# Optimization experiments

Hardware: AMD Instinct MI355X
Metric: run time of the kernel (lower is better)

## Reference

```python
import jax, jax.numpy as jnp
import numpy as np

N = 65536       # active voxels
C = 128         # embed_channels
DEPTH = 4
NSEG = 1024     # number of clusters per level
K = 27          # 3x3x3 kernel taps
LRELU = 0.01
EPS_BN = 1e-5


def _bn(x, g, b):
    # training-mode batchnorm over the voxel axis (biased variance, as torch)
    m = jnp.mean(x, axis=0)
    v = jnp.var(x, axis=0)
    return (x - m) * jax.lax.rsqrt(v + EPS_BN) * g + b


def _lrelu(x):
    return jnp.where(x >= 0, x, LRELU * x)


def _proj(x, w, g, b):
    # Linear(bias=False) -> BatchNorm1d -> LeakyReLU
    return _lrelu(_bn(x @ w, g, b))


def setup_inputs() -> dict:
    key = jax.random.key(0)
    ks = jax.random.split(key, 24)
    s = 1.0 / np.sqrt(C)
    sc = 1.0 / np.sqrt(K * C)
    u = lambda k, shp, sk: jax.random.uniform(k, shp, jnp.float32, -sk, sk)
    g = lambda k, shp: 1.0 + 0.1 * jax.random.normal(k, shp, jnp.float32)
    inp = {}
    inp['feat'] = jax.random.normal(ks[0], (N, C), jnp.float32)
    inp['clusters'] = jax.random.randint(ks[1], (DEPTH - 1, N), 0, NSEG)
    # neighbor table for 3x3x3 sparse conv; value == N means neighbor absent
    inp['neighbor_idx'] = jax.random.randint(ks[2], (N, K), 0, N + 1)
    inp['lw_w'] = u(ks[3], (DEPTH - 1, C, C), s)
    inp['lw_gamma'] = g(ks[4], (DEPTH - 1, C))
    inp['lw_beta'] = 0.1 * jax.random.normal(ks[5], (DEPTH - 1, C), jnp.float32)
    inp['w_w'] = u(ks[6], (DEPTH - 1, C, C), s)
    inp['proj_w'] = u(ks[7], (DEPTH, C, C), s)
    inp['proj_gamma'] = g(ks[8], (DEPTH, C))
    inp['proj_beta'] = 0.1 * jax.random.normal(ks[9], (DEPTH, C), jnp.float32)
    inp['adaptive_w'] = u(ks[10], (C, DEPTH - 1), s)
    inp['fuse_w'] = u(ks[11], (2 * C, C), 1.0 / np.sqrt(2 * C))
    inp['fuse_gamma'] = g(ks[12], (C,))
    inp['fuse_beta'] = 0.1 * jax.random.normal(ks[13], (C,), jnp.float32)
    inp['conv1_w'] = u(ks[14], (K, C, C), sc)
    inp['conv2_w'] = u(ks[15], (K, C, C), sc)
    inp['bn1_gamma'] = g(ks[16], (C,))
    inp['bn1_beta'] = 0.1 * jax.random.normal(ks[17], (C,), jnp.float32)
    inp['bn2_gamma'] = g(ks[18], (C,))
    inp['bn2_beta'] = 0.1 * jax.random.normal(ks[19], (C,), jnp.float32)
    return inp


def _forward(feat, clusters, neighbor_idx, lw_w, lw_gamma, lw_beta, w_w,
             proj_w, proj_gamma, proj_beta, adaptive_w, fuse_w, fuse_gamma,
             fuse_beta, conv1_w, conv2_w, bn1_gamma, bn1_beta, bn2_gamma,
             bn2_beta):
    x_in = feat
    feats = []
    for i in range(DEPTH - 1):
        c = clusters[i]
        pw = _proj(feat, lw_w[i], lw_gamma[i], lw_beta[i])          # [N,C]
        cnt = jnp.maximum(
            jax.ops.segment_sum(jnp.ones((N,), feat.dtype), c, num_segments=NSEG), 1.0)
        seg_mean = jax.ops.segment_sum(pw, c, num_segments=NSEG) / cnt[:, None]
        pw = pw - seg_mean[c]                                        # center per cluster
        pw = pw @ w_w[i]
        pw = jnp.exp(pw - jnp.max(pw))                               # global max, as in source
        pw = pw / (jax.ops.segment_sum(pw, c, num_segments=NSEG)[c] + 1e-6)
        pf = _proj(feat, proj_w[i], proj_gamma[i], proj_beta[i]) * pw
        feats.append(jax.ops.segment_sum(pf, c, num_segments=NSEG)[c])
    adp = jax.nn.softmax(feat @ adaptive_w, axis=1)                  # [N,3]
    feats = jnp.stack(feats, axis=1)                                 # [N,3,C]
    agg = jnp.einsum('ld,ldc->lc', adp, feats)                       # [N,C]
    f_last = _proj(feat, proj_w[DEPTH - 1], proj_gamma[DEPTH - 1], proj_beta[DEPTH - 1])
    fused = _proj(jnp.concatenate([f_last, agg], axis=1), fuse_w, fuse_gamma, fuse_beta) + x_in
    residual = fused
    # 3x3x3 sparse conv on fixed topology: 27 masked gathers + per-tap GEMM
    mask = (neighbor_idx < N).astype(fused.dtype)                    # [N,K]
    idx = jnp.minimum(neighbor_idx, N - 1)

    def sconv(x, w):
        out = jnp.zeros((N, C), x.dtype)
        for k in range(K):
            out = out + (jnp.take(x, idx[:, k], axis=0) * mask[:, k:k + 1]) @ w[k]
        return out

    d = _lrelu(_bn(sconv(fused, conv1_w), bn1_gamma, bn1_beta))
    d = _lrelu(_bn(sconv(d, conv2_w), bn2_gamma, bn2_beta) + residual)
    return d


def reference(feat, clusters, neighbor_idx, lw_w, lw_gamma, lw_beta, w_w,
              proj_w, proj_gamma, proj_beta, adaptive_w, fuse_w, fuse_gamma,
              fuse_beta, conv1_w, conv2_w, bn1_gamma, bn1_beta, bn2_gamma,
              bn2_beta):
    return _forward(feat, clusters, neighbor_idx, lw_w, lw_gamma, lw_beta,
                    w_w, proj_w, proj_gamma, proj_beta, adaptive_w, fuse_w,
                    fuse_gamma, fuse_beta, conv1_w, conv2_w, bn1_gamma,
                    bn1_beta, bn2_gamma, bn2_beta)
```

## Files before the change

### kernel.cpp

```cpp
#include <hip/hip_runtime.h>

typedef unsigned short u16;
typedef unsigned int u32;
typedef __attribute__((ext_vector_type(8))) short bf16x8;
typedef __attribute__((ext_vector_type(4))) float f32x4;
typedef __attribute__((ext_vector_type(4))) u32 u32x4;

#define NROWS 65536
#define CCH 128
#define PE ((size_t)65537*128)

__device__ __forceinline__ float bf2f(u16 x){ u32 u=((u32)x)<<16; return __builtin_bit_cast(float,u); }
__device__ __forceinline__ u16 f2bf(float f){ u32 u=__builtin_bit_cast(u32,f); u += 0x7fffu + ((u>>16)&1u); return (u16)(u>>16); }
__device__ __forceinline__ float lrelu(float v){ return v>=0.f? v : 0.01f*v; }
__device__ __forceinline__ u32 fenc(float f){ u32 u=__builtin_bit_cast(u32,f); return (u & 0x80000000u) ? ~u : (u | 0x80000000u); }
__device__ __forceinline__ float fdec(u32 u){ u32 b = (u & 0x80000000u) ? (u ^ 0x80000000u) : ~u; return __builtin_bit_cast(float,b); }

__global__ __launch_bounds__(256) void prep_transpose(
    const float* __restrict__ lw, const float* __restrict__ ww, const float* __restrict__ pj,
    const float* __restrict__ fw, const float* __restrict__ c1, const float* __restrict__ c2,
    u16* __restrict__ WT)
{
  int i = blockIdx.x*256 + threadIdx.x;
  float v;
  if (i < 49152)      { int j=i;        int m=j>>14,e=j&16383,n=e>>7,k=e&127; v=lw[(m<<14)+(k<<7)+n]; }
  else if (i < 98304) { int j=i-49152;  int m=j>>14,e=j&16383,n=e>>7,k=e&127; v=ww[(m<<14)+(k<<7)+n]; }
  else if (i < 163840){ int j=i-98304;  int m=j>>14,e=j&16383,n=e>>7,k=e&127; v=pj[(m<<14)+(k<<7)+n]; }
  else if (i < 196608){ int j=i-163840; int n=j>>8, k=j&255;                  v=fw[(k<<7)+n]; }
  else if (i < 638976){ int j=i-196608; int m=j>>14,e=j&16383,n=e>>7,k=e&127; v=c1[(m<<14)+(k<<7)+n]; }
  else                { int j=i-638976; int m=j>>14,e=j&16383,n=e>>7,k=e&127; v=c2[(m<<14)+(k<<7)+n]; }
  WT[i]=f2bf(v);
}

__global__ __launch_bounds__(256) void nbrT_k(const int* __restrict__ nbr, int* __restrict__ nbrT){
  __shared__ int s[64*27];
  int b = blockIdx.x;
  for (int i=threadIdx.x; i<64*27; i+=256) s[i] = nbr[b*64*27 + i];
  __syncthreads();
  for (int i=threadIdx.x; i<64*27; i+=256){
    int tap=i>>6, row=i&63;
    nbrT[(size_t)tap*NROWS + b*64 + row] = s[row*27 + tap];
  }
}

__global__ __launch_bounds__(256) void hist_k(const int* __restrict__ cl, int* __restrict__ cnt){
  int i = blockIdx.x*256 + threadIdx.x;
  int l = i>>16;
  atomicAdd(&cnt[l*1024 + cl[i]], 1);
}
__global__ __launch_bounds__(1024) void scan_k(const int* __restrict__ cnt, int* __restrict__ starts, int* __restrict__ cur){
  int l = blockIdx.x, t = threadIdx.x;
  __shared__ int s[1024];
  int v = cnt[l*1024+t];
  s[t]=v; __syncthreads();
  for (int off=1; off<1024; off<<=1){
    int u_ = (t>=off) ? s[t-off] : 0;
    __syncthreads();
    s[t] += u_;
    __syncthreads();
  }
  int incl=s[t], excl=incl-v;
  starts[l*1025+t]=excl;
  if (t==1023) starts[l*1025+1024]=incl;
  cur[l*1024+t]=excl;
}
__global__ __launch_bounds__(256) void scatter_k(const int* __restrict__ cl, int* __restrict__ cur, int* __restrict__ order){
  int i = blockIdx.x*256 + threadIdx.x;
  int l = i>>16;
  int c = cl[i];
  int p = atomicAdd(&cur[l*1024+c], 1);
  order[l*65536 + p] = i & 65535;
}

struct BS7 { const u16* BT[7]; u16* out[7]; float* stats[7]; };

__global__ __launch_bounds__(256,2) void gemm_feat7(const float* __restrict__ feat, BS7 p)
{
  const int tid=threadIdx.x, lane=tid&63, quad=lane>>4, l15=lane&15;
  const int w=tid>>6, rh=w>>1, chq=w&1;
  const int row0=blockIdx.x*128;

  __shared__ __align__(16) u16 ldsA[128*136];
  __shared__ float cs[256];

  #pragma unroll
  for (int it=0; it<8; ++it){
    int row = it*16 + (tid>>4), chn = tid&15;
    const float* Af = feat + (size_t)(row0+row)*CCH + chn*8;
    float4 lo = *(const float4*)(Af);
    float4 hi = *(const float4*)(Af+4);
    u32x4 d;
    d[0]=(u32)f2bf(lo.x)|((u32)f2bf(lo.y)<<16);
    d[1]=(u32)f2bf(lo.z)|((u32)f2bf(lo.w)<<16);
    d[2]=(u32)f2bf(hi.x)|((u32)f2bf(hi.y)<<16);
    d[3]=(u32)f2bf(hi.z)|((u32)f2bf(hi.w)<<16);
    *(u32x4*)(&ldsA[row*136 + chn*8]) = d;
  }
  __syncthreads();

  #pragma unroll 1
  for (int y=0; y<7; ++y){
    const u16* Bb = p.BT[y];
    f32x4 acc[4][4];
    #pragma unroll
    for (int a_=0;a_<4;++a_)
      #pragma unroll
      for (int b_=0;b_<4;++b_) acc[a_][b_]=(f32x4){0.f,0.f,0.f,0.f};
    #pragma unroll
    for (int ks=0; ks<4; ++ks){
      bf16x8 af[4], bfv[4];
      #pragma unroll
      for (int mb=0;mb<4;++mb)
        af[mb]=*(const bf16x8*)(&ldsA[(rh*64+mb*16+l15)*136 + ks*32 + quad*8]);
      #pragma unroll
      for (int nb=0;nb<4;++nb)
        bfv[nb]=*(const bf16x8*)(Bb + (size_t)(chq*64+nb*16+l15)*CCH + ks*32 + quad*8);
      #pragma unroll
      for (int mb=0;mb<4;++mb)
        #pragma unroll
        for (int nb=0;nb<4;++nb)
          acc[mb][nb]=__builtin_amdgcn_mfma_f32_16x16x32_bf16(af[mb],bfv[nb],acc[mb][nb],0,0,0);
    }
    u16* O = p.out[y];
    #pragma unroll
    for (int mb=0;mb<4;++mb){
      int rbase=row0+rh*64+mb*16+quad*4;
      #pragma unroll
      for (int e=0;e<4;++e)
        #pragma unroll
        for (int nb=0;nb<4;++nb)
          O[(size_t)(rbase+e)*CCH + chq*64+nb*16+l15]=f2bf(acc[mb][nb][e]);
    }
    __syncthreads();
    cs[tid]=0.f;
    __syncthreads();
    #pragma unroll
    for (int nb=0;nb<4;++nb){
      float s=0.f,s2=0.f;
      #pragma unroll
      for (int mb=0;mb<4;++mb)
        #pragma unroll
        for (int e=0;e<4;++e){ float v=acc[mb][nb][e]; s+=v; s2+=v*v; }
      s += __shfl_xor(s,16);  s += __shfl_xor(s,32);
      s2+= __shfl_xor(s2,16); s2+= __shfl_xor(s2,32);
      if (lane<16){
        int col=chq*64+nb*16+l15;
        atomicAdd(&cs[col],s); atomicAdd(&cs[128+col],s2);
      }
    }
    __syncthreads();
    atomicAdd(&p.stats[y][tid], cs[tid]);
  }
}

__global__ __launch_bounds__(256) void seg_sum_all(
    const u16* __restrict__ pbase, const float* __restrict__ stats,
    const float* __restrict__ gamma, const float* __restrict__ beta,
    const int* __restrict__ starts, const int* __restrict__ order,
    u16* __restrict__ segmean)
{
  __shared__ float sc[128], sh[128], ssum[128];
  const int tid=threadIdx.x, b=blockIdx.x;
  const int level=b>>10, seg=b&1023;
  const u16* praw = pbase + (size_t)level*PE;
  const float* st = stats + level*256;
  if (tid<128){
    float s=st[tid], s2=st[128+tid];
    float mean=s*(1.0f/65536.0f);
    float var =s2*(1.0f/65536.0f)-mean*mean;
    float rstd=rsqrtf(var+1e-5f);
    float scv =gamma[level*128+tid]*rstd;
    sc[tid]=scv; sh[tid]=beta[level*128+tid]-mean*scv;
    ssum[tid]=0.f;
  }
  __syncthreads();
  const int s0=starts[level*1025+seg], en=starts[level*1025+seg+1];
  const int c2=tid&63, half=tid>>6;
  const int* ord = order + level*65536;
  const float sc0=sc[2*c2], sc1=sc[2*c2+1], sh0=sh[2*c2], sh1=sh[2*c2+1];
  float a0=0.f, a1=0.f;
  for (int m=s0+half; m<en; m+=4){
    int r=ord[m];
    u32 x=*(const u32*)(praw + (size_t)r*CCH + 2*c2);
    a0 += lrelu(sc0*bf2f((u16)(x&0xffffu))+sh0);
    a1 += lrelu(sc1*bf2f((u16)(x>>16))    +sh1);
  }
  atomicAdd(&ssum[2*c2],a0); atomicAdd(&ssum[2*c2+1],a1);
  __syncthreads();
  if (tid<128){
    float inv = 1.0f/fmaxf((float)(en-s0),1.0f);
    segmean[(size_t)b*128+tid]=f2bf(ssum[tid]*inv);
  }
}

__global__ __launch_bounds__(256,2) void gemm_mean(
    const u16* __restrict__ segmean, const u16* __restrict__ wwT, u16* __restrict__ segW)
{
  const int tid=threadIdx.x, lane=tid&63, quad=lane>>4, l15=lane&15;
  const int w=tid>>6, rh=w>>1, chq=w&1;
  const int row0=blockIdx.x*128;
  const int level=row0>>10;
  __shared__ __align__(16) u16 ldsA[128*136];
  #pragma unroll
  for (int it=0; it<8; ++it){
    int row = it*16 + (tid>>4), chn = tid&15;
    *(u32x4*)(&ldsA[row*136 + chn*8]) = *(const u32x4*)(segmean + (size_t)(row0+row)*CCH + chn*8);
  }
  __syncthreads();
  const u16* Bb = wwT + level*16384;
  f32x4 acc[4][4];
  #pragma unroll
  for (int a_=0;a_<4;++a_)
    #pragma unroll
    for (int b_=0;b_<4;++b_) acc[a_][b_]=(f32x4){0.f,0.f,0.f,0.f};
  #pragma unroll
  for (int ks=0; ks<4; ++ks){
    bf16x8 af[4], bfv[4];
    #pragma unroll
    for (int mb=0;mb<4;++mb)
      af[mb]=*(const bf16x8*)(&ldsA[(rh*64+mb*16+l15)*136 + ks*32 + quad*8]);
    #pragma unroll
    for (int nb=0;nb<4;++nb)
      bfv[nb]=*(const bf16x8*)(Bb + (size_t)(chq*64+nb*16+l15)*CCH + ks*32 + quad*8);
    #pragma unroll
    for (int mb=0;mb<4;++mb)
      #pragma unroll
      for (int nb=0;nb<4;++nb)
        acc[mb][nb]=__builtin_amdgcn_mfma_f32_16x16x32_bf16(af[mb],bfv[nb],acc[mb][nb],0,0,0);
  }
  #pragma unroll
  for (int mb=0;mb<4;++mb){
    int rbase=row0+rh*64+mb*16+quad*4;
    #pragma unroll
    for (int e=0;e<4;++e)
      #pragma unroll
      for (int nb=0;nb<4;++nb)
        segW[(size_t)(rbase+e)*CCH + chq*64+nb*16+l15]=f2bf(acc[mb][nb][e]);
  }
}

struct LG { const u16* A[3]; float* out[3]; };
__global__ __launch_bounds__(256,2) void gemm_logits(
    LG p, const u16* __restrict__ wwT,
    const float* __restrict__ stats, const float* __restrict__ lwg, const float* __restrict__ lwb,
    const int* __restrict__ clusters, const u16* __restrict__ segW,
    u32* __restrict__ gmax)
{
  const int tid=threadIdx.x, lane=tid&63, quad=lane>>4, l15=lane&15;
  const int w=tid>>6, rh=w>>1, chq=w&1;
  const int row0=blockIdx.x*128;
  const int y=blockIdx.y;

  __shared__ __align__(16) u16 ldsA[128*136];
  __shared__ float tsc[128], tsh[128];
  __shared__ float wred[4];

  if (tid<128){
    const float* st = stats + y*256;
    float s=st[tid], s2=st[128+tid];
    float mean=s*(1.0f/65536.0f);
    float var =s2*(1.0f/65536.0f)-mean*mean;
    float rstd=rsqrtf(var+1e-5f);
    float scv =lwg[y*128+tid]*rstd;
    tsc[tid]=scv; tsh[tid]=lwb[y*128+tid]-mean*scv;
  }
  __syncthreads();

  const u16* Ab = p.A[y];
  #pragma unroll
  for (int it=0; it<8; ++it){
    int row = it*16 + (tid>>4), chn = tid&15;
    u32x4 d = *(const u32x4*)(Ab + (size_t)(row0+row)*CCH + chn*8);
    #pragma unroll
    for (int pq=0;pq<4;++pq){
      u32 xv=d[pq]; int k=chn*8+2*pq;
      float f0=lrelu(tsc[k  ]*bf2f((u16)(xv&0xffffu))+tsh[k  ]);
      float f1=lrelu(tsc[k+1]*bf2f((u16)(xv>>16))    +tsh[k+1]);
      d[pq]=(u32)f2bf(f0)|((u32)f2bf(f1)<<16);
    }
    *(u32x4*)(&ldsA[row*136 + chn*8]) = d;
  }
  __syncthreads();

  const u16* Bb = wwT + y*16384;
  f32x4 acc[4][4];
  #pragma unroll
  for (int a_=0;a_<4;++a_)
    #pragma unroll
    for (int b_=0;b_<4;++b_) acc[a_][b_]=(f32x4){0.f,0.f,0.f,0.f};
  #pragma unroll
  for (int ks=0; ks<4; ++ks){
    bf16x8 af[4], bfv[4];
    #pragma unroll
    for (int mb=0;mb<4;++mb)
      af[mb]=*(const bf16x8*)(&ldsA[(rh*64+mb*16+l15)*136 + ks*32 + quad*8]);
    #pragma unroll
    for (int nb=0;nb<4;++nb)
      bfv[nb]=*(const bf16x8*)(Bb + (size_t)(chq*64+nb*16+l15)*CCH + ks*32 + quad*8);
    #pragma unroll
    for (int mb=0;mb<4;++mb)
      #pragma unroll
      for (int nb=0;nb<4;++nb)
        acc[mb][nb]=__builtin_amdgcn_mfma_f32_16x16x32_bf16(af[mb],bfv[nb],acc[mb][nb],0,0,0);
  }
  float* O = p.out[y];
  float m=-3.0e38f;
  #pragma unroll
  for (int mb=0;mb<4;++mb){
    int rbase=row0+rh*64+mb*16+quad*4;
    #pragma unroll
    for (int e=0;e<4;++e){
      int row=rbase+e;
      int cl=clusters[(size_t)y*NROWS + row];
      const u16* sw = segW + ((size_t)(y*1024+cl))*CCH;
      #pragma unroll
      for (int nb=0;nb<4;++nb){
        int col=chq*64+nb*16+l15;
        float v=acc[mb][nb][e]-bf2f(sw[col]);
        O[(size_t)row*CCH + col]=v;
        m=fmaxf(m,v);
      }
    }
  }
  #pragma unroll
  for (int o=1;o<64;o<<=1) m=fmaxf(m,__shfl_xor(m,o));
  if (lane==0) wred[w]=m;
  __syncthreads();
  if (tid==0){
    float mm=fmaxf(fmaxf(wred[0],wred[1]),fmaxf(wred[2],wred[3]));
    atomicMax(&gmax[y], fenc(mm));
  }
}

__global__ __launch_bounds__(256,2) void gemm_fuse(
    const u16* __restrict__ A0, const u16* __restrict__ A1,
    const float* __restrict__ tstat, const float* __restrict__ tg, const float* __restrict__ tb,
    const u16* __restrict__ BT, u16* __restrict__ out, float* __restrict__ stats)
{
  const int tid=threadIdx.x, lane=tid&63, quad=lane>>4, l15=lane&15;
  const int w=tid>>6, rh=w>>1, chq=w&1;
  const int row0=blockIdx.x*128;

  __shared__ __align__(16) u16 ldsA[128*136];
  __shared__ float tsc[128], tsh[128];
  __shared__ float cs[256];

  if (tid<128){
    float s=tstat[tid], s2=tstat[128+tid];
    float mean=s*(1.0f/65536.0f);
    float var =s2*(1.0f/65536.0f)-mean*mean;
    float rstd=rsqrtf(var+1e-5f);
    float scv =tg[tid]*rstd;
    tsc[tid]=scv; tsh[tid]=tb[tid]-mean*scv;
  }

  f32x4 acc[4][4];
  #pragma unroll
  for (int a_=0;a_<4;++a_)
    #pragma unroll
    for (int b_=0;b_<4;++b_) acc[a_][b_]=(f32x4){0.f,0.f,0.f,0.f};

  #pragma unroll 1
  for (int tap=0; tap<2; ++tap){
    __syncthreads();
    const u16* Ab = tap ? A1 : A0;
    #pragma unroll
    for (int it=0; it<8; ++it){
      int row = it*16 + (tid>>4), chn = tid&15;
      u32x4 d = *(const u32x4*)(Ab + (size_t)(row0+row)*CCH + chn*8);
      if (tap==0){
        #pragma unroll
        for (int pq=0;pq<4;++pq){
          u32 xv=d[pq]; int k=chn*8+2*pq;
          float f0=lrelu(tsc[k  ]*bf2f((u16)(xv&0xffffu))+tsh[k  ]);
          float f1=lrelu(tsc[k+1]*bf2f((u16)(xv>>16))    +tsh[k+1]);
          d[pq]=(u32)f2bf(f0)|((u32)f2bf(f1)<<16);
        }
      }
      *(u32x4*)(&ldsA[row*136 + chn*8]) = d;
    }
    __syncthreads();
    const u16* Bb = BT + tap*128;
    #pragma unroll
    for (int ks=0; ks<4; ++ks){
      bf16x8 af[4], bfv[4];
      #pragma unroll
      for (int mb=0;mb<4;++mb)
        af[mb]=*(const bf16x8*)(&ldsA[(rh*64+mb*16+l15)*136 + ks*32 + quad*8]);
      #pragma unroll
      for (int nb=0;nb<4;++nb)
        bfv[nb]=*(const bf16x8*)(Bb + (size_t)(chq*64+nb*16+l15)*256 + ks*32 + quad*8);
      #pragma unroll
      for (int mb=0;mb<4;++mb)
        #pragma unroll
        for (int nb=0;nb<4;++nb)
          acc[mb][nb]=__builtin_amdgcn_mfma_f32_16x16x32_bf16(af[mb],bfv[nb],acc[mb][nb],0,0,0);
    }
  }
  #pragma unroll
  for (int mb=0;mb<4;++mb){
    int rbase=row0+rh*64+mb*16+quad*4;
    #pragma unroll
    for (int e=0;e<4;++e)
      #pragma unroll
      for (int nb=0;nb<4;++nb)
        out[(size_t)(rbase+e)*CCH + chq*64+nb*16+l15]=f2bf(acc[mb][nb][e]);
  }
  __syncthreads();
  cs[tid]=0.f;
  __syncthreads();
  #pragma unroll
  for (int nb=0;nb<4;++nb){
    float s=0.f,s2=0.f;
    #pragma unroll
    for (int mb=0;mb<4;++mb)
      #pragma unroll
      for (int e=0;e<4;++e){ float v=acc[mb][nb][e]; s+=v; s2+=v*v; }
    s += __shfl_xor(s,16);  s += __shfl_xor(s,32);
    s2+= __shfl_xor(s2,16); s2+= __shfl_xor(s2,32);
    if (lane<16){
      int col=chq*64+nb*16+l15;
      atomicAdd(&cs[col],s); atomicAdd(&cs[128+col],s2);
    }
  }
  __syncthreads();
  atomicAdd(&stats[tid], cs[tid]);
}

template<bool TRANSA>
__device__ __forceinline__ u32x4 conv_xf(u32x4 d, int ar, int schn,
                                         const float* tsc, const float* tsh)
{
  if (TRANSA){
    if (ar >= NROWS) return (u32x4){0u,0u,0u,0u};
    #pragma unroll
    for (int p=0;p<4;++p){
      u32 xv=d[p]; int k=schn*8+2*p;
      float f0=lrelu(tsc[k  ]*bf2f((u16)(xv&0xffffu))+tsh[k  ]);
      float f1=lrelu(tsc[k+1]*bf2f((u16)(xv>>16))    +tsh[k+1]);
      d[p]=(u32)f2bf(f0)|((u32)f2bf(f1)<<16);
    }
  }
  return d;
}

template<bool TRANSA>
__device__ __forceinline__ void conv_tap(
    int tap, int cur,
    const u16* __restrict__ A, const u16* __restrict__ BT, const int* __restrict__ nbrT,
    int row0, int srow, int schn, int rh, int chq, int quad, int l15,
    u16 (&bufA)[2][128*136],
    u32x4 (&preC)[8], int (&ixC)[8], u32x4 (&preN)[8], int (&ixN)[8],
    f32x4 (&acc)[4][4], const float* tsc, const float* tsh)
{
  if (tap < 25){
    #pragma unroll
    for (int it=0; it<8; ++it){
      int ar = nbrT[(size_t)(tap+2)*NROWS + row0 + it*16 + srow];
      ixN[it]=ar;
      preN[it] = *(const u32x4*)(A + (size_t)ar*CCH + schn*8);
    }
  }
  const u16* Bb = BT + tap*16384;
  #pragma unroll
  for (int ks=0; ks<4; ++ks){
    bf16x8 af[4], bfv[4];
    #pragma unroll
    for (int mb=0;mb<4;++mb)
      af[mb]=*(const bf16x8*)(&bufA[cur][(rh*64+mb*16+l15)*136 + ks*32 + quad*8]);
    #pragma unroll
    for (int nb=0;nb<4;++nb)
      bfv[nb]=*(const bf16x8*)(Bb + (size_t)(chq*64+nb*16+l15)*CCH + ks*32 + quad*8);
    #pragma unroll
    for (int mb=0;mb<4;++mb)
      #pragma unroll
      for (int nb=0;nb<4;++nb)
        acc[mb][nb]=__builtin_amdgcn_mfma_f32_16x16x32_bf16(af[mb],bfv[nb],acc[mb][nb],0,0,0);
  }
  if (tap < 26){
    const int nxt = cur^1;
    #pragma unroll
    for (int it=0; it<8; ++it)
      *(u32x4*)(&bufA[nxt][(it*16+srow)*136 + schn*8]) = conv_xf<TRANSA>(preC[it], ixC[it], schn, tsc, tsh);
  }
  __syncthreads();
}

template<bool TRANSA>
__global__ __launch_bounds__(256,2) void conv_k(
    const u16* __restrict__ A, const u16* __restrict__ BT,
    const int* __restrict__ nbrT, u16* __restrict__ out, float* __restrict__ stats,
    const float* __restrict__ tstat, const float* __restrict__ tg, const float* __restrict__ tb)
{
  const int tid=threadIdx.x, lane=tid&63, quad=lane>>4, l15=lane&15;
  const int w=tid>>6, rh=w>>1, chq=w&1;
  const int row0=blockIdx.x*128;
  const int srow=tid>>4, schn=tid&15;

  __shared__ __align__(16) u16 bufA[2][128*136];
  __shared__ float cs[256];
  __shared__ float tsc[128], tsh[128];

  if (TRANSA){
    if (tid<128){
      float s=tstat[tid], s2=tstat[128+tid];
      float mean=s*(1.0f/65536.0f);
      float var =s2*(1.0f/65536.0f)-mean*mean;
      float rstd=rsqrtf(var+1e-5f);
      float scv =tg[tid]*rstd;
      tsc[tid]=scv; tsh[tid]=tb[tid]-mean*scv;
    }
    __syncthreads();
  }

  u32x4 pre0[8], pre1[8];
  int   ix0[8],  ix1[8];

  {
    u32x4 t0[8]; int i0[8];
    #pragma unroll
    for (int it=0; it<8; ++it){
      i0[it] = nbrT[row0 + it*16 + srow];
      t0[it] = *(const u32x4*)(A + (size_t)i0[it]*CCH + schn*8);
    }
    #pragma unroll
    for (int it=0; it<8; ++it){
      ix0[it] = nbrT[(size_t)NROWS + row0 + it*16 + srow];
      pre0[it] = *(const u32x4*)(A + (size_t)ix0[it]*CCH + schn*8);
    }
    #pragma unroll
    for (int it=0; it<8; ++it)
      *(u32x4*)(&bufA[0][(it*16+srow)*136 + schn*8]) = conv_xf<TRANSA>(t0[it], i0[it], schn, tsc, tsh);
  }
  __syncthreads();

  f32x4 acc[4][4];
  #pragma unroll
  for (int a_=0;a_<4;++a_)
    #pragma unroll
    for (int b_=0;b_<4;++b_) acc[a_][b_]=(f32x4){0.f,0.f,0.f,0.f};

  #pragma unroll 1
  for (int t2=0; t2<13; ++t2){
    conv_tap<TRANSA>(2*t2,   0, A,BT,nbrT,row0,srow,schn,rh,chq,quad,l15,bufA,pre0,ix0,pre1,ix1,acc,tsc,tsh);
    conv_tap<TRANSA>(2*t2+1, 1, A,BT,nbrT,row0,srow,schn,rh,chq,quad,l15,bufA,pre1,ix1,pre0,ix0,acc,tsc,tsh);
  }
  conv_tap<TRANSA>(26, 0, A,BT,nbrT,row0,srow,schn,rh,chq,quad,l15,bufA,pre0,ix0,pre1,ix1,acc,tsc,tsh);

  #pragma unroll
  for (int mb=0;mb<4;++mb){
    int rbase=row0+rh*64+mb*16+quad*4;
    #pragma unroll
    for (int e=0;e<4;++e)
      #pragma unroll
      for (int nb=0;nb<4;++nb)
        out[(size_t)(rbase+e)*CCH + chq*64+nb*16+l15]=f2bf(acc[mb][nb][e]);
  }
  cs[tid]=0.f;
  __syncthreads();
  #pragma unroll
  for (int nb=0;nb<4;++nb){
    float s=0.f,s2=0.f;
    #pragma unroll
    for (int mb=0;mb<4;++mb)
      #pragma unroll
      for (int e=0;e<4;++e){ float v=acc[mb][nb][e]; s+=v; s2+=v*v; }
    s += __shfl_xor(s,16);  s += __shfl_xor(s,32);
    s2+= __shfl_xor(s2,16); s2+= __shfl_xor(s2,32);
    if (lane<16){
      int col=chq*64+nb*16+l15;
      atomicAdd(&cs[col],s); atomicAdd(&cs[128+col],s2);
    }
  }
  __syncthreads();
  atomicAdd(&stats[tid], cs[tid]);
}

struct F3 { const float* f[3]; };
__global__ __launch_bounds__(256) void seg_softmax_all(
    F3 pw2s, const u16* __restrict__ pfbase,
    const float* __restrict__ stats, const float* __restrict__ gamma, const float* __restrict__ beta,
    const u32* __restrict__ gmax,
    const int* __restrict__ starts, const int* __restrict__ order,
    float* __restrict__ segpf)
{
  __shared__ float sc[128], sh[128], se[128], spf[128];
  const int tid=threadIdx.x, b=blockIdx.x;
  const int level=b>>10, seg=b&1023;
  const float* pw2 = pw2s.f[level];
  const u16* pfraw = pfbase + (size_t)level*PE;
  const float* st = stats + level*256;
  if (tid<128){
    float s=st[tid], s2=st[128+tid];
    float mean=s*(1.0f/65536.0f);
    float var =s2*(1.0f/65536.0f)-mean*mean;
    float rstd=rsqrtf(var+1e-5f);
    float scv =gamma[level*128+tid]*rstd;
    sc[tid]=scv; sh[tid]=beta[level*128+tid]-mean*scv;
    se[tid]=0.f; spf[tid]=0.f;
  }
  __syncthreads();
  const float M = fdec(gmax[level]);
  const int s0=starts[level*1025+seg], en=starts[level*1025+seg+1];
  const int c2=tid&63, half=tid>>6;
  const int* ord = order + level*65536;
  float a0=0.f, a1=0.f;
  for (int m=s0+half; m<en; m+=4){
    int r=ord[m];
    float2 x=*(const float2*)(pw2 + (size_t)r*CCH + 2*c2);
    a0 += __expf(x.x-M); a1 += __expf(x.y-M);
  }
  atomicAdd(&se[2*c2],a0); atomicAdd(&se[2*c2+1],a1);
  __syncthreads();
  const float d0=1.0f/(se[2*c2]+1e-6f), d1=1.0f/(se[2*c2+1]+1e-6f);
  const float sc0=sc[2*c2], sc1=sc[2*c2+1], sh0=sh[2*c2], sh1=sh[2*c2+1];
  float p0=0.f, p1=0.f;
  for (int m=s0+half; m<en; m+=4){
    int r=ord[m];
    float2 x=*(const float2*)(pw2 + (size_t)r*CCH + 2*c2);
    u32 f=*(const u32*)(pfraw + (size_t)r*CCH + 2*c2);
    p0 += lrelu(sc0*bf2f((u16)(f&0xffffu))+sh0) * (__expf(x.x-M)*d0);
    p1 += lrelu(sc1*bf2f((u16)(f>>16))    +sh1) * (__expf(x.y-M)*d1);
  }
  atomicAdd(&spf[2*c2],p0); atomicAdd(&spf[2*c2+1],p1);
  __syncthreads();
  if (tid<128) segpf[(size_t)b*128+tid]=spf[tid];
}

__global__ __launch_bounds__(256) void adp_agg(
    const float* __restrict__ feat, const float* __restrict__ aw,
    const int* __restrict__ clusters, const float* __restrict__ segpf,
    u16* __restrict__ agg)
{
  const int tid=threadIdx.x, w=tid>>6, lane=tid&63;
  const int r = blockIdx.x*4 + w;
  float t0=0.f,t1=0.f,t2=0.f;
  #pragma unroll
  for (int cc=0; cc<2; ++cc){
    int c = lane + cc*64;
    float f=feat[(size_t)r*CCH+c];
    t0 += f*aw[c*3+0];
    t1 += f*aw[c*3+1];
    t2 += f*aw[c*3+2];
  }
  #pragma unroll
  for (int o=1;o<64;o<<=1){
    t0+=__shfl_xor(t0,o); t1+=__shfl_xor(t1,o); t2+=__shfl_xor(t2,o);
  }
  float m=fmaxf(t0,fmaxf(t1,t2));
  float e0=__expf(t0-m), e1=__expf(t1-m), e2=__expf(t2-m);
  float inv=1.0f/(e0+e1+e2);
  float p0=e0*inv,p1=e1*inv,p2=e2*inv;
  int c0=clusters[r], c1_=clusters[NROWS+r], c2_=clusters[2*NROWS+r];
  const float* s0p=segpf + (size_t)c0*128;
  const float* s1p=segpf + (size_t)(1024+c1_)*128;
  const float* s2p=segpf + (size_t)(2048+c2_)*128;
  #pragma unroll
  for (int cc=0; cc<2; ++cc){
    int c = lane + cc*64;
    float v = p0*s0p[c] + p1*s1p[c] + p2*s2p[c];
    agg[(size_t)r*CCH+c]=f2bf(v);
  }
}

__global__ __launch_bounds__(256) void apply_kernel(
    const u16* __restrict__ raw, const float* __restrict__ stats,
    const float* __restrict__ g_, const float* __restrict__ b_,
    const void* __restrict__ resid, int rf32,
    void* __restrict__ out, int of32,
    int nrows, int mode)
{
  __shared__ float sc[128], sh[128];
  const int tid=threadIdx.x;
  if (tid<128){
    float s=stats[tid], s2=stats[128+tid];
    float mean=s*(1.0f/65536.0f);
    float var =s2*(1.0f/65536.0f)-mean*mean;
    float rstd=rsqrtf(var+1e-5f);
    float scv =g_[tid]*rstd;
    sc[tid]=scv; sh[tid]=b_[tid]-mean*scv;
  }
  __syncthreads();
  size_t chunk = (size_t)blockIdx.x*256 + tid;
  size_t total = (size_t)nrows*16;
  if (chunk >= total) return;
  size_t r = chunk>>4; int c8 = (int)(chunk&15)*8;
  float v[8];
  if (r >= NROWS){
    #pragma unroll
    for (int p=0;p<8;++p) v[p]=0.f;
  } else {
    u32x4 x = *(const u32x4*)(raw + r*CCH + c8);
    float rsd[8];
    if (resid){
      if (rf32){
        const float* R = ((const float*)resid) + r*CCH + c8;
        float4 lo=*(const float4*)R, hi=*(const float4*)(R+4);
        rsd[0]=lo.x; rsd[1]=lo.y; rsd[2]=lo.z; rsd[3]=lo.w;
        rsd[4]=hi.x; rsd[5]=hi.y; rsd[6]=hi.z; rsd[7]=hi.w;
      } else {
        u32x4 rv = *(const u32x4*)(((const u16*)resid) + r*CCH + c8);
        #pragma unroll
        for (int p=0;p<4;++p){
          rsd[2*p]  =bf2f((u16)(rv[p]&0xffffu));
          rsd[2*p+1]=bf2f((u16)(rv[p]>>16));
        }
      }
    } else {
      #pragma unroll
      for (int p=0;p<8;++p) rsd[p]=0.f;
    }
    #pragma unroll
    for (int p=0;p<4;++p){
      u32 xv=x[p];
      int k=c8+2*p;
      float v0=sc[k  ]*bf2f((u16)(xv&0xffffu))+sh[k  ];
      float v1=sc[k+1]*bf2f((u16)(xv>>16))    +sh[k+1];
      if (mode==0){ v[2*p]=lrelu(v0)+rsd[2*p]; v[2*p+1]=lrelu(v1)+rsd[2*p+1]; }
      else        { v[2*p]=lrelu(v0+rsd[2*p]); v[2*p+1]=lrelu(v1+rsd[2*p+1]); }
    }
  }
  if (of32){
    float* O = ((float*)out) + r*CCH + c8;
    float4 lo={v[0],v[1],v[2],v[3]}, hi={v[4],v[5],v[6],v[7]};
    *(float4*)O = lo; *(float4*)(O+4) = hi;
  } else {
    u32x4 o;
    #pragma unroll
    for (int p=0;p<4;++p) o[p] = (u32)f2bf(v[2*p]) | ((u32)f2bf(v[2*p+1])<<16);
    *(u32x4*)(((u16*)out) + r*CCH + c8) = o;
  }
}

extern "C" void kernel_launch(void* const* d_in, const int* in_sizes, int n_in,
                              void* d_out, int out_size, void* d_ws, size_t ws_size,
                              hipStream_t stream)
{
  (void)in_sizes; (void)n_in; (void)out_size; (void)ws_size;
  const float* feat = (const float*)d_in[0];
  const int* clusters = (const int*)d_in[1];
  const int* nbr  = (const int*)d_in[2];
  const float* lw_w = (const float*)d_in[3];
  const float* lw_g = (const float*)d_in[4];
  const float* lw_b = (const float*)d_in[5];
  const float* w_w  = (const float*)d_in[6];
  const float* pj_w = (const float*)d_in[7];
  const float* pj_g = (const float*)d_in[8];
  const float* pj_b = (const float*)d_in[9];
  const float* aw   = (const float*)d_in[10];
  const float* fu_w = (const float*)d_in[11];
  const float* fu_g = (const float*)d_in[12];
  const float* fu_b = (const float*)d_in[13];
  const float* c1w  = (const float*)d_in[14];
  const float* c2w  = (const float*)d_in[15];
  const float* b1g  = (const float*)d_in[16];
  const float* b1b  = (const float*)d_in[17];
  const float* b2g  = (const float*)d_in[18];
  const float* b2b  = (const float*)d_in[19];

  char* wsb = (char*)d_ws;
  u16* WT = (u16*)wsb;
  const size_t o_zero = 2162688;
  float* stats = (float*)(wsb + o_zero);
  u32*  gmax   = (u32*) (wsb + o_zero + 10240);
  int*  cnt    = (int*) (wsb + o_zero + 10496);
  int*  cur    = (int*) (wsb + o_zero + 22784);
  u16*  segmean= (u16*) (wsb + o_zero + 35072);
  u16*  segWb  = (u16*) (wsb + o_zero + 35072 + 786432);
  float* segpf = (float*)(wsb + o_zero + 35072);
  const size_t zero_bytes = 22784;
  const size_t o_starts = o_zero + 35072 + (size_t)3*1024*128*4;
  int* starts = (int*)(wsb + o_starts);
  const size_t o_order = o_starts + 12544;
  int* order  = (int*)(wsb + o_order);
  const size_t o_pool = o_order + 786432;
  const size_t PE_B = PE*2;
  u16* A0=(u16*)(wsb+o_pool + 0*PE_B);
  u16* A1=(u16*)(wsb+o_pool + 1*PE_B);
  u16* A2=(u16*)(wsb+o_pool + 2*PE_B);
  u16* A3=(u16*)(wsb+o_pool + 3*PE_B);
  u16* A4=(u16*)(wsb+o_pool + 4*PE_B);
  u16* A5=(u16*)(wsb+o_pool + 5*PE_B);
  u16* A6=(u16*)(wsb+o_pool + 6*PE_B);
  const size_t o_F = o_pool + 7*PE_B;
  float* F0=(float*)(wsb+o_F);
  float* F1=(float*)(wsb+o_F+33554432);
  float* F2=(float*)d_out;
  int* nbrT = (int*)(wsb+o_F);

  hipMemsetAsync(wsb+o_zero, 0, zero_bytes, stream);
  prep_transpose<<<4224,256,0,stream>>>(lw_w,w_w,pj_w,fu_w,c1w,c2w,WT);
  hist_k   <<<768,256,0,stream>>>(clusters, cnt);
  scan_k   <<<3,1024,0,stream>>>(cnt, starts, cur);
  scatter_k<<<768,256,0,stream>>>(clusters, cur, order);

  const u16* lwT = WT;
  const u16* wwT = WT + 49152;
  const u16* pjT = WT + 98304;
  const u16* fuT = WT + 163840;
  const u16* c1T = WT + 196608;
  const u16* c2T = WT + 638976;

  float* stLW=stats;
  float* stPJ=stats+768;
  float* stFU=stats+1792; float* stB1=stats+2048; float* stB2=stats+2304;

  {
    BS7 p;
    for (int i=0;i<3;++i){ p.BT[i]=lwT+i*16384;     p.out[i]=A0+(size_t)i*PE; p.stats[i]=stLW+i*256; }
    for (int i=0;i<4;++i){ p.BT[3+i]=pjT+i*16384;   p.out[3+i]=(i<3)?(A3+(size_t)i*PE):A6; p.stats[3+i]=stPJ+i*256; }
    gemm_feat7<<<512,256,0,stream>>>(feat, p);
  }
  seg_sum_all<<<3072,256,0,stream>>>(A0, stLW, lw_g, lw_b, starts, order, segmean);
  gemm_mean<<<24,256,0,stream>>>(segmean, wwT, segWb);
  {
    LG p;
    float* Fo[3]={F0,F1,F2};
    for (int i=0;i<3;++i){ p.A[i]=A0+(size_t)i*PE; p.out[i]=Fo[i]; }
    gemm_logits<<<dim3(512,3),256,0,stream>>>(p, wwT, stLW, lw_g, lw_b, clusters, segWb, gmax);
  }
  {
    F3 f; f.f[0]=F0; f.f[1]=F1; f.f[2]=F2;
    seg_softmax_all<<<3072,256,0,stream>>>(f, A3, stPJ, pj_g, pj_b, gmax, starts, order, segpf);
  }
  nbrT_k<<<1024,256,0,stream>>>(nbr, nbrT);
  adp_agg<<<16384,256,0,stream>>>(feat, aw, clusters, segpf, A4);
  gemm_fuse<<<512,256,0,stream>>>(A6, A4, stPJ+768, pj_g+384, pj_b+384, fuT, A5, stFU);
  apply_kernel<<<4097,256,0,stream>>>(A5, stFU, fu_g, fu_b, feat, 1, A0, 0, NROWS+1, 0);
  conv_k<false><<<512,256,0,stream>>>(A0, c1T, nbrT, A1, stB1, nullptr, nullptr, nullptr);
  conv_k<true ><<<512,256,0,stream>>>(A1, c2T, nbrT, A3, stB2, stB1, b1g, b1b);
  apply_kernel<<<4096,256,0,stream>>>(A3, stB2, b2g, b2b, A0, 0, (float*)d_out, 1, NROWS, 1);
}
```

Before: 732.7 us.

## Rewrite sparse conv to gather neighbor rows straight into registers, no LDS

The sparse conv kernel no longer stages gathered rows in double-buffered shared memory with per-tap barriers. Each wave now owns 32 rows and loads its gathered A fragments directly into registers from global memory. Index and row loads are prefetched two to three taps ahead, and each wave computes all 128 output channels. The BN1+LeakyReLU transform that used to be fused into the second conv's gather moves into a separate apply_kernel pass that writes an intermediate buffer. This removes LDS traffic and synchronization, but costs more register pressure, repeated B-weight loads per wave, and an extra full read/write pass over the activations.

Result: slower. 988.3 us (+34.9%).

```diff
diff --git a/kernel.cpp b/kernel.cpp
--- a/kernel.cpp
+++ b/kernel.cpp
@@ -427,148 +427,90 @@
   atomicAdd(&stats[tid], cs[tid]);
 }
 
-template<bool TRANSA>
-__device__ __forceinline__ u32x4 conv_xf(u32x4 d, int ar, int schn,
-                                         const float* tsc, const float* tsh)
-{
-  if (TRANSA){
-    if (ar >= NROWS) return (u32x4){0u,0u,0u,0u};
-    #pragma unroll
-    for (int p=0;p<4;++p){
-      u32 xv=d[p]; int k=schn*8+2*p;
-      float f0=lrelu(tsc[k  ]*bf2f((u16)(xv&0xffffu))+tsh[k  ]);
-      float f1=lrelu(tsc[k+1]*bf2f((u16)(xv>>16))    +tsh[k+1]);
-      d[p]=(u32)f2bf(f0)|((u32)f2bf(f1)<<16);
-    }
-  }
-  return d;
-}
-
-template<bool TRANSA>
-__device__ __forceinline__ void conv_tap(
-    int tap, int cur,
-    const u16* __restrict__ A, const u16* __restrict__ BT, const int* __restrict__ nbrT,
-    int row0, int srow, int schn, int rh, int chq, int quad, int l15,
-    u16 (&bufA)[2][128*136],
-    u32x4 (&preC)[8], int (&ixC)[8], u32x4 (&preN)[8], int (&ixN)[8],
-    f32x4 (&acc)[4][4], const float* tsc, const float* tsh)
-{
-  if (tap < 25){
-    #pragma unroll
-    for (int it=0; it<8; ++it){
-      int ar = nbrT[(size_t)(tap+2)*NROWS + row0 + it*16 + srow];
-      ixN[it]=ar;
-      preN[it] = *(const u32x4*)(A + (size_t)ar*CCH + schn*8);
-    }
-  }
-  const u16* Bb = BT + tap*16384;
-  #pragma unroll
-  for (int ks=0; ks<4; ++ks){
-    bf16x8 af[4], bfv[4];
-    #pragma unroll
-    for (int mb=0;mb<4;++mb)
-      af[mb]=*(const bf16x8*)(&bufA[cur][(rh*64+mb*16+l15)*136 + ks*32 + quad*8]);
-    #pragma unroll
-    for (int nb=0;nb<4;++nb)
-      bfv[nb]=*(const bf16x8*)(Bb + (size_t)(chq*64+nb*16+l15)*CCH + ks*32 + quad*8);
-    #pragma unroll
-    for (int mb=0;mb<4;++mb)
-      #pragma unroll
-      for (int nb=0;nb<4;++nb)
-        acc[mb][nb]=__builtin_amdgcn_mfma_f32_16x16x32_bf16(af[mb],bfv[nb],acc[mb][nb],0,0,0);
-  }
-  if (tap < 26){
-    const int nxt = cur^1;
-    #pragma unroll
-    for (int it=0; it<8; ++it)
-      *(u32x4*)(&bufA[nxt][(it*16+srow)*136 + schn*8]) = conv_xf<TRANSA>(preC[it], ixC[it], schn, tsc, tsh);
-  }
-  __syncthreads();
-}
-
-template<bool TRANSA>
 __global__ __launch_bounds__(256,2) void conv_k(
     const u16* __restrict__ A, const u16* __restrict__ BT,
-    const int* __restrict__ nbrT, u16* __restrict__ out, float* __restrict__ stats,
-    const float* __restrict__ tstat, const float* __restrict__ tg, const float* __restrict__ tb)
+    const int* __restrict__ nbrT, u16* __restrict__ out, float* __restrict__ stats)
 {
   const int tid=threadIdx.x, lane=tid&63, quad=lane>>4, l15=lane&15;
-  const int w=tid>>6, rh=w>>1, chq=w&1;
-  const int row0=blockIdx.x*128;
-  const int srow=tid>>4, schn=tid&15;
-
-  __shared__ __align__(16) u16 bufA[2][128*136];
+  const int wv=tid>>6;
+  const int row0 = blockIdx.x*128 + wv*32;
   __shared__ float cs[256];
-  __shared__ float tsc[128], tsh[128];
-
-  if (TRANSA){
-    if (tid<128){
-      float s=tstat[tid], s2=tstat[128+tid];
-      float mean=s*(1.0f/65536.0f);
-      float var =s2*(1.0f/65536.0f)-mean*mean;
-      float rstd=rsqrtf(var+1e-5f);
-      float scv =tg[tid]*rstd;
-      tsc[tid]=scv; tsh[tid]=tb[tid]-mean*scv;
-    }
-    __syncthreads();
-  }
-
-  u32x4 pre0[8], pre1[8];
-  int   ix0[8],  ix1[8];
-
-  {
-    u32x4 t0[8]; int i0[8];
-    #pragma unroll
-    for (int it=0; it<8; ++it){
-      i0[it] = nbrT[row0 + it*16 + srow];
-      t0[it] = *(const u32x4*)(A + (size_t)i0[it]*CCH + schn*8);
-    }
-    #pragma unroll
-    for (int it=0; it<8; ++it){
-      ix0[it] = nbrT[(size_t)NROWS + row0 + it*16 + srow];
-      pre0[it] = *(const u32x4*)(A + (size_t)ix0[it]*CCH + schn*8);
-    }
-    #pragma unroll
-    for (int it=0; it<8; ++it)
-      *(u32x4*)(&bufA[0][(it*16+srow)*136 + schn*8]) = conv_xf<TRANSA>(t0[it], i0[it], schn, tsc, tsh);
-  }
-  __syncthreads();
-
-  f32x4 acc[4][4];
-  #pragma unroll
-  for (int a_=0;a_<4;++a_)
-    #pragma unroll
-    for (int b_=0;b_<4;++b_) acc[a_][b_]=(f32x4){0.f,0.f,0.f,0.f};
-
-  #pragma unroll 1
-  for (int t2=0; t2<13; ++t2){
-    conv_tap<TRANSA>(2*t2,   0, A,BT,nbrT,row0,srow,schn,rh,chq,quad,l15,bufA,pre0,ix0,pre1,ix1,acc,tsc,tsh);
-    conv_tap<TRANSA>(2*t2+1, 1, A,BT,nbrT,row0,srow,schn,rh,chq,quad,l15,bufA,pre1,ix1,pre0,ix0,acc,tsc,tsh);
-  }
-  conv_tap<TRANSA>(26, 0, A,BT,nbrT,row0,srow,schn,rh,chq,quad,l15,bufA,pre0,ix0,pre1,ix1,acc,tsc,tsh);
-
-  #pragma unroll
-  for (int mb=0;mb<4;++mb){
-    int rbase=row0+rh*64+mb*16+quad*4;
+
+  f32x4 acc[2][8];
+  #pragma unroll
+  for (int mb=0;mb<2;++mb)
+    #pragma unroll
+    for (int nb=0;nb<8;++nb) acc[mb][nb]=(f32x4){0.f,0.f,0.f,0.f};
+
+  bf16x8 af[3][2][4];
+  int idx[3][2];
+
+  #pragma unroll
+  for (int s=0;s<3;++s)
+    #pragma unroll
+    for (int mb=0;mb<2;++mb)
+      idx[s][mb] = nbrT[(size_t)s*NROWS + row0 + mb*16 + l15];
+  #pragma unroll
+  for (int s=0;s<2;++s)
+    #pragma unroll
+    for (int mb=0;mb<2;++mb){
+      const u16* rp = A + (size_t)idx[s][mb]*CCH + quad*8;
+      #pragma unroll
+      for (int ks=0;ks<4;++ks)
+        af[s][mb][ks] = *(const bf16x8*)(rp + ks*32);
+    }
+
+  #pragma unroll 27
+  for (int t=0; t<27; ++t){
+    if (t+3<27){
+      #pragma unroll
+      for (int mb=0;mb<2;++mb)
+        idx[(t+3)%3][mb] = nbrT[(size_t)(t+3)*NROWS + row0 + mb*16 + l15];
+    }
+    if (t+2<27){
+      #pragma unroll
+      for (int mb=0;mb<2;++mb){
+        const u16* rp = A + (size_t)idx[(t+2)%3][mb]*CCH + quad*8;
+        #pragma unroll
+        for (int ks=0;ks<4;++ks)
+          af[(t+2)%3][mb][ks] = *(const bf16x8*)(rp + ks*32);
+      }
+    }
+    const u16* Bb = BT + t*16384;
+    #pragma unroll
+    for (int ks=0;ks<4;++ks){
+      #pragma unroll
+      for (int nb=0;nb<8;++nb){
+        bf16x8 bfv = *(const bf16x8*)(Bb + (size_t)(nb*16+l15)*CCH + ks*32 + quad*8);
+        acc[0][nb]=__builtin_amdgcn_mfma_f32_16x16x32_bf16(af[t%3][0][ks],bfv,acc[0][nb],0,0,0);
+        acc[1][nb]=__builtin_amdgcn_mfma_f32_16x16x32_bf16(af[t%3][1][ks],bfv,acc[1][nb],0,0,0);
+      }
+    }
+  }
+
+  #pragma unroll
+  for (int mb=0;mb<2;++mb){
+    int rbase = row0 + mb*16 + quad*4;
     #pragma unroll
     for (int e=0;e<4;++e)
       #pragma unroll
-      for (int nb=0;nb<4;++nb)
-        out[(size_t)(rbase+e)*CCH + chq*64+nb*16+l15]=f2bf(acc[mb][nb][e]);
-  }
+      for (int nb=0;nb<8;++nb)
+        out[(size_t)(rbase+e)*CCH + nb*16+l15]=f2bf(acc[mb][nb][e]);
+  }
+
   cs[tid]=0.f;
   __syncthreads();
   #pragma unroll
-  for (int nb=0;nb<4;++nb){
+  for (int nb=0;nb<8;++nb){
     float s=0.f,s2=0.f;
     #pragma unroll
-    for (int mb=0;mb<4;++mb)
+    for (int mb=0;mb<2;++mb)
       #pragma unroll
       for (int e=0;e<4;++e){ float v=acc[mb][nb][e]; s+=v; s2+=v*v; }
     s += __shfl_xor(s,16);  s += __shfl_xor(s,32);
     s2+= __shfl_xor(s2,16); s2+= __shfl_xor(s2,32);
     if (lane<16){
-      int col=chq*64+nb*16+l15;
+      int col=nb*16+l15;
       atomicAdd(&cs[col],s); atomicAdd(&cs[128+col],s2);
     }
   }
@@ -827,7 +769,8 @@
   adp_agg<<<16384,256,0,stream>>>(feat, aw, clusters, segpf, A4);
   gemm_fuse<<<512,256,0,stream>>>(A6, A4, stPJ+768, pj_g+384, pj_b+384, fuT, A5, stFU);
   apply_kernel<<<4097,256,0,stream>>>(A5, stFU, fu_g, fu_b, feat, 1, A0, 0, NROWS+1, 0);
-  conv_k<false><<<512,256,0,stream>>>(A0, c1T, nbrT, A1, stB1, nullptr, nullptr, nullptr);
-  conv_k<true ><<<512,256,0,stream>>>(A1, c2T, nbrT, A3, stB2, stB1, b1g, b1b);
+  conv_k<<<512,256,0,stream>>>(A0, c1T, nbrT, A1, stB1);
+  apply_kernel<<<4097,256,0,stream>>>(A1, stB1, b1g, b1b, nullptr, 0, A2, 0, NROWS+1, 0);
+  conv_k<<<512,256,0,stream>>>(A2, c2T, nbrT, A3, stB2);
   apply_kernel<<<4096,256,0,stream>>>(A3, stB2, b2g, b2b, A0, 0, (float*)d_out, 1, NROWS, 1);
 }
```
